# Kernel tuning notes

Hardware: AMD Instinct MI355X
Metric: run time of the kernel (lower is better)

## Reference

```python
import jax, jax.numpy as jnp
import numpy as np

H = 256          # hidden_dim from config
B, S = 128, 2048 # batch, seq_len
D_CTX, D_RFX = 6, 2


def setup_inputs() -> dict:
    key = jax.random.key(0)
    ks = jax.random.split(key, 16)
    def lin(k, out_d, in_d):
        # torch nn.Linear default init: U(-1/sqrt(in_d), 1/sqrt(in_d))
        bound = 1.0 / np.sqrt(in_d)
        k1, k2 = jax.random.split(k)
        w = jax.random.uniform(k1, (out_d, in_d), jnp.float32, -bound, bound)
        b = jax.random.uniform(k2, (out_d,), jnp.float32, -bound, bound)
        return w, b
    x = jax.random.normal(ks[0], (B, S, D_CTX), jnp.float32)
    # GRUCell params (torch layout: rows ordered [reset, update, new])
    bnd = 1.0 / np.sqrt(H)
    w_ih = jax.random.uniform(ks[1], (3 * H, D_CTX), jnp.float32, -bnd, bnd)
    w_hh = jax.random.uniform(ks[2], (3 * H, H), jnp.float32, -bnd, bnd)
    b_ih = jax.random.uniform(ks[3], (3 * H,), jnp.float32, -bnd, bnd)
    b_hh = jax.random.uniform(ks[4], (3 * H,), jnp.float32, -bnd, bnd)
    w_gain, b_gain = lin(ks[5], D_RFX, H)
    w_bias, b_bias = lin(ks[6], 4, H)
    w_reflex, b_reflex = lin(ks[7], H, D_RFX)
    w_policy, b_policy = lin(ks[8], 2, H)
    w_motor, b_motor = lin(ks[9], 2, H)
    return dict(x=x, w_ih=w_ih, w_hh=w_hh, b_ih=b_ih, b_hh=b_hh,
                w_gain=w_gain, b_gain=b_gain, w_bias=w_bias, b_bias=b_bias,
                w_reflex=w_reflex, b_reflex=b_reflex,
                w_policy=w_policy, b_policy=b_policy,
                w_motor=w_motor, b_motor=b_motor)


def _forward(x, w_ih, w_hh, b_ih, b_hh, w_gain, b_gain, w_bias, b_bias,
             w_reflex, b_reflex, w_policy, b_policy, w_motor, b_motor):
    # x_context == cat(x[:,:,0:2], x[:,:,2:3], x[:,:,3:6]) == x itself
    x_reflex = x[:, :, 0:2]
    # Precompute input contribution to all 3 GRU gates: [B, S, 3H]
    gates_x = jnp.einsum('bsd,gd->bsg', x, w_ih) + b_ih
    gates_x_t = jnp.swapaxes(gates_x, 0, 1)     # [S, B, 3H]
    x_reflex_t = jnp.swapaxes(x_reflex, 0, 1)   # [S, B, 2]

    h0 = jnp.zeros((x.shape[0], H), x.dtype)

    def step(h, inp):
        gi, xr = inp
        gh = h @ w_hh.T + b_hh
        r = jax.nn.sigmoid(gi[:, :H] + gh[:, :H])
        z = jax.nn.sigmoid(gi[:, H:2 * H] + gh[:, H:2 * H])
        n = jnp.tanh(gi[:, 2 * H:] + r * gh[:, 2 * H:])
        h_new = (1.0 - z) * n + z * h
        gain = jax.nn.sigmoid(h_new @ w_gain.T + b_gain)   # [B,2]
        bias = h_new @ w_bias.T + b_bias                    # [B,4]
        feat = jax.nn.relu((xr * gain) @ w_reflex.T + b_reflex)  # [B,H]
        probs = feat @ w_policy.T + b_policy + bias[:, 0:2]
        dirs = jnp.tanh(feat @ w_motor.T + b_motor + bias[:, 2:4])
        y = jnp.concatenate([probs, dirs], axis=1)          # [B,4]
        return h_new, (y, h_new)

    _, (y_t, h_t) = jax.lax.scan(step, h0, (gates_x_t, x_reflex_t))
    y_pred = jnp.swapaxes(y_t, 0, 1)          # [B,S,4]
    router_activity = jnp.swapaxes(h_t, 0, 1) # [B,S,H]
    return y_pred, router_activity


def reference(x, w_ih, w_hh, b_ih, b_hh, w_gain, b_gain, w_bias, b_bias,
              w_reflex, b_reflex, w_policy, b_policy, w_motor, b_motor):
    return _forward(x, w_ih, w_hh, b_ih, b_hh, w_gain, b_gain, w_bias, b_bias,
                    w_reflex, b_reflex, w_policy, b_policy, w_motor, b_motor)
```

## Files before the change

### kernel.cpp

```cpp
#include <hip/hip_runtime.h>
#include <cstdint>
#include <cstddef>

#define Hn 256
#define Sn 2048
#define Bn 128
#define NT 1024

typedef _Float16 half2_t __attribute__((ext_vector_type(2)));

__device__ __forceinline__ float fdot2_(half2_t a, half2_t b, float c){
#if __has_builtin(__builtin_amdgcn_fdot2)
  return __builtin_amdgcn_fdot2(a, b, c, false);
#else
  float d;
  asm volatile("v_dot2_f32_f16 %0, %1, %2, %3" : "=v"(d) : "v"(a), "v"(b), "v"(c));
  return d;
#endif
}

__device__ __forceinline__ float qsum_(float v){
  int x = __builtin_bit_cast(int, v);
  int y = __builtin_amdgcn_mov_dpp(x, 0xB1, 0xF, 0xF, true);
  v += __builtin_bit_cast(float, y);
  x = __builtin_bit_cast(int, v);
  y = __builtin_amdgcn_mov_dpp(x, 0x4E, 0xF, 0xF, true);
  return v + __builtin_bit_cast(float, y);
}

__device__ __forceinline__ float rfl_(float v){
  return __builtin_bit_cast(float, __builtin_amdgcn_readfirstlane(__builtin_bit_cast(int, v)));
}

__device__ __forceinline__ float sigmoid_(float v){ return 1.0f/(1.0f+__expf(-v)); }
__device__ __forceinline__ float tanh_(float v){
  float e = __expf(-2.0f*__builtin_fabsf(v));
  float r = (1.0f-e)/(1.0f+e);
  return __builtin_copysignf(r, v);
}

__global__ void
__attribute__((amdgpu_flat_work_group_size(NT, NT), amdgpu_waves_per_eu(4, 4)))
bio_rnn(const float* __restrict__ x,
        const float* __restrict__ w_ih, const float* __restrict__ w_hh,
        const float* __restrict__ b_ih, const float* __restrict__ b_hh,
        const float* __restrict__ w_gain, const float* __restrict__ b_gain,
        const float* __restrict__ w_bias, const float* __restrict__ b_bias,
        const float* __restrict__ w_reflex, const float* __restrict__ b_reflex,
        const float* __restrict__ w_policy, const float* __restrict__ b_policy,
        const float* __restrict__ w_motor, const float* __restrict__ b_motor,
        float* __restrict__ y_out, float* __restrict__ router)
{
  const int b  = blockIdx.x;
  const int t  = threadIdx.x;
  const int kq = t & 3;
  const int j  = t >> 2;

  __shared__ __align__(16) unsigned char hraw[4*160];
  __shared__ float PRE[4][Hn];
  __shared__ float REDp[4][8];
  __shared__ float REDq[4][4];
  __shared__ float HW[13][Hn];
  __shared__ float SB[10];

  half2_t w0[32], w1[32], w2[32];
  {
    const float* p0 = w_hh + (size_t)(j       )*Hn + kq*64;
    const float* p1 = w_hh + (size_t)(j +   Hn)*Hn + kq*64;
    const float* p2 = w_hh + (size_t)(j + 2*Hn)*Hn + kq*64;
    #pragma unroll
    for (int m = 0; m < 32; m++){
      half2_t a; a.x=(_Float16)p0[2*m]; a.y=(_Float16)p0[2*m+1]; w0[m]=a;
      half2_t c; c.x=(_Float16)p1[2*m]; c.y=(_Float16)p1[2*m+1]; w1[m]=c;
      half2_t d; d.x=(_Float16)p2[2*m]; d.y=(_Float16)p2[2*m+1]; w2[m]=d;
    }
  }
  half2_t wi0, wi1, wi2; float bd0, bd1, bd2, bd3;
  {
    half2_t z; z.x=(_Float16)0.f; z.y=(_Float16)0.f;
    wi0=z; wi1=z; wi2=z; bd0=bd1=bd2=bd3=0.f;
    if (kq < 3){
      wi0.x=(_Float16)w_ih[(size_t)(j       )*6+2*kq]; wi0.y=(_Float16)w_ih[(size_t)(j       )*6+2*kq+1];
      wi1.x=(_Float16)w_ih[(size_t)(j +   Hn)*6+2*kq]; wi1.y=(_Float16)w_ih[(size_t)(j +   Hn)*6+2*kq+1];
      wi2.x=(_Float16)w_ih[(size_t)(j + 2*Hn)*6+2*kq]; wi2.y=(_Float16)w_ih[(size_t)(j + 2*Hn)*6+2*kq+1];
    } else {
      bd0 = b_ih[j]      + b_hh[j];
      bd1 = b_ih[j+Hn]   + b_hh[j+Hn];
      bd2 = b_hh[j+2*Hn];
      bd3 = b_ih[j+2*Hn];
    }
  }
  if (t < Hn){
    HW[0][t] = w_gain[t];        HW[1][t]  = w_gain[Hn + t];
    HW[2][t] = w_bias[t];        HW[3][t]  = w_bias[Hn + t];
    HW[4][t] = w_bias[2*Hn + t]; HW[5][t]  = w_bias[3*Hn + t];
    HW[6][t] = w_reflex[2*t];    HW[7][t]  = w_reflex[2*t + 1];
    HW[8][t] = b_reflex[t];
    HW[9][t] = w_policy[t];      HW[10][t] = w_policy[Hn + t];
    HW[11][t] = w_motor[t];      HW[12][t] = w_motor[Hn + t];
  }
  if (t < 160) ((unsigned int*)hraw)[t] = 0u;
  if (t == 0){
    SB[0]=b_gain[0]; SB[1]=b_gain[1];
    SB[2]=b_bias[0]; SB[3]=b_bias[1]; SB[4]=b_bias[2]; SB[5]=b_bias[3];
    SB[6]=b_policy[0]; SB[7]=b_policy[1]; SB[8]=b_motor[0]; SB[9]=b_motor[1];
  }
  float hprev = 0.f;
  __syncthreads();

  const float* xp   = x      + (size_t)b * Sn * 6;
  float* rbase      = router + (size_t)b * Sn * Hn;
  const uint4* hc   = (const uint4*)(hraw + kq*160);

  for (int s = 0; s < Sn; s++){
    const float x0=rfl_(xp[0]), x1=rfl_(xp[1]), x2=rfl_(xp[2]);
    const float x3=rfl_(xp[3]), x4=rfl_(xp[4]), x5=rfl_(xp[5]);
    float xa = (kq==0)?x0:((kq==1)?x2:x4);
    float xb = (kq==0)?x1:((kq==1)?x3:x5);
    half2_t xpk; xpk.x=(_Float16)xa; xpk.y=(_Float16)xb;

    float a0=bd0, a1=bd1, a2=bd2, a3=bd3;
    a0 = fdot2_(wi0, xpk, a0);
    a1 = fdot2_(wi1, xpk, a1);
    a3 = fdot2_(wi2, xpk, a3);

    #pragma unroll
    for (int i = 0; i < 8; i++){
      uint4 hv = hc[i];
      half2_t h0 = __builtin_bit_cast(half2_t, hv.x);
      half2_t h1 = __builtin_bit_cast(half2_t, hv.y);
      half2_t h2 = __builtin_bit_cast(half2_t, hv.z);
      half2_t h3 = __builtin_bit_cast(half2_t, hv.w);
      a0=fdot2_(w0[4*i+0],h0,a0); a1=fdot2_(w1[4*i+0],h0,a1); a2=fdot2_(w2[4*i+0],h0,a2);
      a0=fdot2_(w0[4*i+1],h1,a0); a1=fdot2_(w1[4*i+1],h1,a1); a2=fdot2_(w2[4*i+1],h1,a2);
      a0=fdot2_(w0[4*i+2],h2,a0); a1=fdot2_(w1[4*i+2],h2,a1); a2=fdot2_(w2[4*i+2],h2,a2);
      a0=fdot2_(w0[4*i+3],h3,a0); a1=fdot2_(w1[4*i+3],h3,a1); a2=fdot2_(w2[4*i+3],h3,a2);
    }
    a0 = qsum_(a0); a1 = qsum_(a1); a2 = qsum_(a2); a3 = qsum_(a3);
    if (kq == 0){ PRE[0][j]=a0; PRE[1][j]=a1; PRE[2][j]=a2; PRE[3][j]=a3; }
    __syncthreads();

    if (t < Hn){
      float pr = PRE[0][t], pz = PRE[1][t], pg = PRE[2][t], pn = PRE[3][t];
      float r = sigmoid_(pr);
      float z = sigmoid_(pz);
      float n = tanh_(pn + r*pg);
      float h = (1.f - z)*n + z*hprev;
      hprev = h;
      *(_Float16*)(hraw + (t>>6)*160 + (t&63)*2) = (_Float16)h;
      rbase[(size_t)s*Hn + t] = h;
      float p0=h*HW[0][t], p1=h*HW[1][t], p2=h*HW[2][t];
      float p3=h*HW[3][t], p4=h*HW[4][t], p5=h*HW[5][t];
      #pragma unroll
      for (int off = 32; off >= 1; off >>= 1){
        p0 += __shfl_xor(p0, off); p1 += __shfl_xor(p1, off); p2 += __shfl_xor(p2, off);
        p3 += __shfl_xor(p3, off); p4 += __shfl_xor(p4, off); p5 += __shfl_xor(p5, off);
      }
      if ((t & 63) == 0){
        const int wv = t >> 6;
        REDp[wv][0]=p0; REDp[wv][1]=p1; REDp[wv][2]=p2;
        REDp[wv][3]=p3; REDp[wv][4]=p4; REDp[wv][5]=p5;
      }
    }
    __syncthreads();
    if (t < Hn){
      float g0 = REDp[0][0]+REDp[1][0]+REDp[2][0]+REDp[3][0] + SB[0];
      float g1 = REDp[0][1]+REDp[1][1]+REDp[2][1]+REDp[3][1] + SB[1];
      g0 = sigmoid_(g0); g1 = sigmoid_(g1);
      float f = (x0*g0)*HW[6][t] + (x1*g1)*HW[7][t] + HW[8][t];
      f = fmaxf(f, 0.f);
      float q0=f*HW[9][t], q1=f*HW[10][t], q2=f*HW[11][t], q3=f*HW[12][t];
      #pragma unroll
      for (int off = 32; off >= 1; off >>= 1){
        q0 += __shfl_xor(q0, off); q1 += __shfl_xor(q1, off);
        q2 += __shfl_xor(q2, off); q3 += __shfl_xor(q3, off);
      }
      if ((t & 63) == 0){
        const int wv = t >> 6;
        REDq[wv][0]=q0; REDq[wv][1]=q1; REDq[wv][2]=q2; REDq[wv][3]=q3;
      }
    }
    __syncthreads();
    if (t == 0){
      float s0 = REDq[0][0]+REDq[1][0]+REDq[2][0]+REDq[3][0];
      float s1 = REDq[0][1]+REDq[1][1]+REDq[2][1]+REDq[3][1];
      float s2 = REDq[0][2]+REDq[1][2]+REDq[2][2]+REDq[3][2];
      float s3 = REDq[0][3]+REDq[1][3]+REDq[2][3]+REDq[3][3];
      float B0 = REDp[0][2]+REDp[1][2]+REDp[2][2]+REDp[3][2] + SB[2];
      float B1 = REDp[0][3]+REDp[1][3]+REDp[2][3]+REDp[3][3] + SB[3];
      float B2 = REDp[0][4]+REDp[1][4]+REDp[2][4]+REDp[3][4] + SB[4];
      float B3 = REDp[0][5]+REDp[1][5]+REDp[2][5]+REDp[3][5] + SB[5];
      float4 o;
      o.x = s0 + SB[6] + B0;
      o.y = s1 + SB[7] + B1;
      o.z = tanh_(s2 + SB[8] + B2);
      o.w = tanh_(s3 + SB[9] + B3);
      *(float4*)(y_out + (size_t)b * Sn * 4 + (size_t)s * 4) = o;
    }
    xp += 6;
  }
}

extern "C" void kernel_launch(void* const* d_in, const int* in_sizes, int n_in,
                              void* d_out, int out_size, void* d_ws, size_t ws_size,
                              hipStream_t stream)
{
  const float* x        = (const float*)d_in[0];
  const float* w_ih     = (const float*)d_in[1];
  const float* w_hh     = (const float*)d_in[2];
  const float* b_ih     = (const float*)d_in[3];
  const float* b_hh     = (const float*)d_in[4];
  const float* w_gain   = (const float*)d_in[5];
  const float* b_gain   = (const float*)d_in[6];
  const float* w_bias   = (const float*)d_in[7];
  const float* b_bias   = (const float*)d_in[8];
  const float* w_reflex = (const float*)d_in[9];
  const float* b_reflex = (const float*)d_in[10];
  const float* w_policy = (const float*)d_in[11];
  const float* b_policy = (const float*)d_in[12];
  const float* w_motor  = (const float*)d_in[13];
  const float* b_motor  = (const float*)d_in[14];

  float* y_out  = (float*)d_out;
  float* router = (float*)d_out + (size_t)Bn * Sn * 4;

  bio_rnn<<<dim3(Bn), dim3(NT), 0, stream>>>(
      x, w_ih, w_hh, b_ih, b_hh, w_gain, b_gain, w_bias, b_bias,
      w_reflex, b_reflex, w_policy, b_policy, w_motor, b_motor,
      y_out, router);
}
```

Before: 6.333 ms.

## Assign one full W_hh row per thread with 768-thread blocks instead of quad split

Reworks the recurrent matvec so each of 768 threads owns one complete gate row of W_hh (128 half2 in registers) instead of four threads splitting a row and combining with DPP reductions. The h state is packed contiguously in LDS and broadcast-read by all threads, and the input projection for the n gate goes to a separate shared array. This removes the per-step cross-lane quad reductions and the redundant bias/input lanes. In exchange it needs more registers per thread (VGPR cap raised to 168, waves per EU lowered to 3) and a serial 128-step dot chain split into four accumulators per thread.

```diff
diff --git a/kernel.cpp b/kernel.cpp
--- a/kernel.cpp
+++ b/kernel.cpp
@@ -5,7 +5,7 @@
 #define Hn 256
 #define Sn 2048
 #define Bn 128
-#define NT 1024
+#define NT 768
 
 typedef _Float16 half2_t __attribute__((ext_vector_type(2)));
 
@@ -19,15 +19,6 @@
 #endif
 }
 
-__device__ __forceinline__ float qsum_(float v){
-  int x = __builtin_bit_cast(int, v);
-  int y = __builtin_amdgcn_mov_dpp(x, 0xB1, 0xF, 0xF, true);
-  v += __builtin_bit_cast(float, y);
-  x = __builtin_bit_cast(int, v);
-  y = __builtin_amdgcn_mov_dpp(x, 0x4E, 0xF, 0xF, true);
-  return v + __builtin_bit_cast(float, y);
-}
-
 __device__ __forceinline__ float rfl_(float v){
   return __builtin_bit_cast(float, __builtin_amdgcn_readfirstlane(__builtin_bit_cast(int, v)));
 }
@@ -40,7 +31,9 @@
 }
 
 __global__ void
-__attribute__((amdgpu_flat_work_group_size(NT, NT), amdgpu_waves_per_eu(4, 4)))
+__attribute__((amdgpu_flat_work_group_size(NT, NT),
+               amdgpu_waves_per_eu(3, 3),
+               amdgpu_num_vgpr(168)))
 bio_rnn(const float* __restrict__ x,
         const float* __restrict__ w_ih, const float* __restrict__ w_hh,
         const float* __restrict__ b_ih, const float* __restrict__ b_hh,
@@ -51,45 +44,36 @@
         const float* __restrict__ w_motor, const float* __restrict__ b_motor,
         float* __restrict__ y_out, float* __restrict__ router)
 {
-  const int b  = blockIdx.x;
-  const int t  = threadIdx.x;
-  const int kq = t & 3;
-  const int j  = t >> 2;
-
-  __shared__ __align__(16) unsigned char hraw[4*160];
-  __shared__ float PRE[4][Hn];
+  const int b = blockIdx.x;
+  const int t = threadIdx.x;
+
+  __shared__ __align__(16) half2_t hpk[Hn/2];
+  __shared__ float A[NT];
+  __shared__ float GIN[Hn];
   __shared__ float REDp[4][8];
   __shared__ float REDq[4][4];
   __shared__ float HW[13][Hn];
   __shared__ float SB[10];
 
-  half2_t w0[32], w1[32], w2[32];
+  half2_t w[128];
   {
-    const float* p0 = w_hh + (size_t)(j       )*Hn + kq*64;
-    const float* p1 = w_hh + (size_t)(j +   Hn)*Hn + kq*64;
-    const float* p2 = w_hh + (size_t)(j + 2*Hn)*Hn + kq*64;
+    const float* wr = w_hh + (size_t)t * Hn;
     #pragma unroll
-    for (int m = 0; m < 32; m++){
-      half2_t a; a.x=(_Float16)p0[2*m]; a.y=(_Float16)p0[2*m+1]; w0[m]=a;
-      half2_t c; c.x=(_Float16)p1[2*m]; c.y=(_Float16)p1[2*m+1]; w1[m]=c;
-      half2_t d; d.x=(_Float16)p2[2*m]; d.y=(_Float16)p2[2*m+1]; w2[m]=d;
-    }
-  }
-  half2_t wi0, wi1, wi2; float bd0, bd1, bd2, bd3;
+    for (int k = 0; k < 128; k++){
+      half2_t v; v.x = (_Float16)wr[2*k]; v.y = (_Float16)wr[2*k+1];
+      w[k] = v;
+    }
+  }
+  half2_t wi0, wi1, wi2;
   {
-    half2_t z; z.x=(_Float16)0.f; z.y=(_Float16)0.f;
-    wi0=z; wi1=z; wi2=z; bd0=bd1=bd2=bd3=0.f;
-    if (kq < 3){
-      wi0.x=(_Float16)w_ih[(size_t)(j       )*6+2*kq]; wi0.y=(_Float16)w_ih[(size_t)(j       )*6+2*kq+1];
-      wi1.x=(_Float16)w_ih[(size_t)(j +   Hn)*6+2*kq]; wi1.y=(_Float16)w_ih[(size_t)(j +   Hn)*6+2*kq+1];
-      wi2.x=(_Float16)w_ih[(size_t)(j + 2*Hn)*6+2*kq]; wi2.y=(_Float16)w_ih[(size_t)(j + 2*Hn)*6+2*kq+1];
-    } else {
-      bd0 = b_ih[j]      + b_hh[j];
-      bd1 = b_ih[j+Hn]   + b_hh[j+Hn];
-      bd2 = b_hh[j+2*Hn];
-      bd3 = b_ih[j+2*Hn];
-    }
-  }
+    const float* wr = w_ih + (size_t)t * 6;
+    wi0.x=(_Float16)wr[0]; wi0.y=(_Float16)wr[1];
+    wi1.x=(_Float16)wr[2]; wi1.y=(_Float16)wr[3];
+    wi2.x=(_Float16)wr[4]; wi2.y=(_Float16)wr[5];
+  }
+  const float bias_h = b_hh[t];
+  const float bias_i = b_ih[t];
+
   if (t < Hn){
     HW[0][t] = w_gain[t];        HW[1][t]  = w_gain[Hn + t];
     HW[2][t] = w_bias[t];        HW[3][t]  = w_bias[Hn + t];
@@ -99,7 +83,7 @@
     HW[9][t] = w_policy[t];      HW[10][t] = w_policy[Hn + t];
     HW[11][t] = w_motor[t];      HW[12][t] = w_motor[Hn + t];
   }
-  if (t < 160) ((unsigned int*)hraw)[t] = 0u;
+  if (t < Hn/2){ half2_t z0; z0.x=(_Float16)0.f; z0.y=(_Float16)0.f; hpk[t] = z0; }
   if (t == 0){
     SB[0]=b_gain[0]; SB[1]=b_gain[1];
     SB[2]=b_bias[0]; SB[3]=b_bias[1]; SB[4]=b_bias[2]; SB[5]=b_bias[3];
@@ -108,47 +92,41 @@
   float hprev = 0.f;
   __syncthreads();
 
-  const float* xp   = x      + (size_t)b * Sn * 6;
-  float* rbase      = router + (size_t)b * Sn * Hn;
-  const uint4* hc   = (const uint4*)(hraw + kq*160);
+  const float* xp = x      + (size_t)b * Sn * 6;
+  float* rbase    = router + (size_t)b * Sn * Hn;
+  const uint4* hv4 = (const uint4*)hpk;
 
   for (int s = 0; s < Sn; s++){
     const float x0=rfl_(xp[0]), x1=rfl_(xp[1]), x2=rfl_(xp[2]);
     const float x3=rfl_(xp[3]), x4=rfl_(xp[4]), x5=rfl_(xp[5]);
-    float xa = (kq==0)?x0:((kq==1)?x2:x4);
-    float xb = (kq==0)?x1:((kq==1)?x3:x5);
-    half2_t xpk; xpk.x=(_Float16)xa; xpk.y=(_Float16)xb;
-
-    float a0=bd0, a1=bd1, a2=bd2, a3=bd3;
-    a0 = fdot2_(wi0, xpk, a0);
-    a1 = fdot2_(wi1, xpk, a1);
-    a3 = fdot2_(wi2, xpk, a3);
-
+    half2_t xq0, xq1, xq2;
+    xq0.x=(_Float16)x0; xq0.y=(_Float16)x1;
+    xq1.x=(_Float16)x2; xq1.y=(_Float16)x3;
+    xq2.x=(_Float16)x4; xq2.y=(_Float16)x5;
+    float gx = fdot2_(wi2, xq2, fdot2_(wi1, xq1, fdot2_(wi0, xq0, bias_i)));
+
+    float a0 = bias_h, a1 = 0.f, a2 = 0.f, a3 = 0.f;
     #pragma unroll
-    for (int i = 0; i < 8; i++){
-      uint4 hv = hc[i];
-      half2_t h0 = __builtin_bit_cast(half2_t, hv.x);
-      half2_t h1 = __builtin_bit_cast(half2_t, hv.y);
-      half2_t h2 = __builtin_bit_cast(half2_t, hv.z);
-      half2_t h3 = __builtin_bit_cast(half2_t, hv.w);
-      a0=fdot2_(w0[4*i+0],h0,a0); a1=fdot2_(w1[4*i+0],h0,a1); a2=fdot2_(w2[4*i+0],h0,a2);
-      a0=fdot2_(w0[4*i+1],h1,a0); a1=fdot2_(w1[4*i+1],h1,a1); a2=fdot2_(w2[4*i+1],h1,a2);
-      a0=fdot2_(w0[4*i+2],h2,a0); a1=fdot2_(w1[4*i+2],h2,a1); a2=fdot2_(w2[4*i+2],h2,a2);
-      a0=fdot2_(w0[4*i+3],h3,a0); a1=fdot2_(w1[4*i+3],h3,a1); a2=fdot2_(w2[4*i+3],h3,a2);
-    }
-    a0 = qsum_(a0); a1 = qsum_(a1); a2 = qsum_(a2); a3 = qsum_(a3);
-    if (kq == 0){ PRE[0][j]=a0; PRE[1][j]=a1; PRE[2][j]=a2; PRE[3][j]=a3; }
+    for (int k = 0; k < 32; k++){
+      uint4 hv = hv4[k];
+      a0 = fdot2_(w[4*k+0], __builtin_bit_cast(half2_t, hv.x), a0);
+      a1 = fdot2_(w[4*k+1], __builtin_bit_cast(half2_t, hv.y), a1);
+      a2 = fdot2_(w[4*k+2], __builtin_bit_cast(half2_t, hv.z), a2);
+      a3 = fdot2_(w[4*k+3], __builtin_bit_cast(half2_t, hv.w), a3);
+    }
+    float acc = (a0 + a1) + (a2 + a3);
+    if (t < 512) A[t] = acc + gx;
+    else { A[t] = acc; GIN[t - 512] = gx; }
     __syncthreads();
 
     if (t < Hn){
-      float pr = PRE[0][t], pz = PRE[1][t], pg = PRE[2][t], pn = PRE[3][t];
-      float r = sigmoid_(pr);
-      float z = sigmoid_(pz);
-      float n = tanh_(pn + r*pg);
-      float h = (1.f - z)*n + z*hprev;
+      float r = sigmoid_(A[t]);
+      float z = sigmoid_(A[t + Hn]);
+      float n = tanh_(GIN[t] + r * A[t + 2*Hn]);
+      float h = (1.f - z) * n + z * hprev;
       hprev = h;
-      *(_Float16*)(hraw + (t>>6)*160 + (t&63)*2) = (_Float16)h;
-      rbase[(size_t)s*Hn + t] = h;
+      ((_Float16*)hpk)[t] = (_Float16)h;
+      rbase[(size_t)s * Hn + t] = h;
       float p0=h*HW[0][t], p1=h*HW[1][t], p2=h*HW[2][t];
       float p3=h*HW[3][t], p4=h*HW[4][t], p5=h*HW[5][t];
       #pragma unroll
```

Measured after the change: 6.662 ms. +5.2%, slower.
